# Performance work log

Hardware: AMD Instinct MI355X
Metric: run time of the kernel (lower is better)

Reference implementation:

```python
import jax, jax.numpy as jnp
import numpy as np

B, L, D, H = 4, 2048, 1024, 16
HD = D // H

def setup_inputs() -> dict:
    key = jax.random.key(0)
    k1, k2, k3, k4 = jax.random.split(key, 4)
    return {
        "Q": jax.random.normal(k1, (B, L, D), dtype=jnp.float32),
        "K": jax.random.normal(k2, (B, L, D), dtype=jnp.float32),
        "V": jax.random.normal(k3, (B, L, D), dtype=jnp.float32),
        "W_out": jax.random.normal(k4, (D, D), dtype=jnp.float32) * (1.0 / np.sqrt(D)),
        "b_out": jnp.zeros((D,), dtype=jnp.float32),
    }

def reference(Q, K, V, W_out, b_out):
    b, l, d = Q.shape
    h, hd = H, d // H
    q = Q.reshape(b, l, h, hd)
    k = K.reshape(b, l, h, hd)
    v = V.reshape(b, l, h, hd)
    # energy: [b, h, q, k]
    energy = jnp.einsum('nqhd,nkhd->nhqk', q, k)
    # NOTE: original scales by sqrt(embed_dim), not sqrt(head_dim)
    attn = jax.nn.softmax(energy / jnp.sqrt(jnp.float32(d)), axis=-1)
    out = jnp.einsum('nhql,nlhd->nqhd', attn, v).reshape(b, l, d)
    # torch nn.Linear: x @ W.T + b
    return out @ W_out.T + b_out
```

## Files before the change

kernel.cpp:

```cpp
#include <hip/hip_runtime.h>
#include <hip/hip_bf16.h>


#define B_  4
#define L_  2048
#define D_  1024
#define H_  16

typedef float  f32x4  __attribute__((ext_vector_type(4)));
typedef short  bf16x8 __attribute__((ext_vector_type(8)));
typedef short  bf16x4 __attribute__((ext_vector_type(4)));

__device__ inline unsigned short f2bf(float x) {
    union { float f; unsigned u; } v; v.f = x;
    unsigned r = v.u + 0x7FFFu + ((v.u >> 16) & 1u);
    return (unsigned short)(r >> 16);
}
__device__ inline unsigned pack_rne2(float lo, float hi) {
    return (unsigned)f2bf(lo) | ((unsigned)f2bf(hi) << 16);
}
__device__ inline unsigned pack_trunc2(float lo, float hi) {
    union { float f; unsigned u; } a, b; a.f = lo; b.f = hi;
    return (a.u >> 16) | (b.u & 0xFFFF0000u);
}
__device__ inline float fast_exp2(float x) {
#if __has_builtin(__builtin_amdgcn_exp2f)
    return __builtin_amdgcn_exp2f(x);
#else
    return exp2f(x);
#endif
}
__device__ inline bf16x8 pack8s(float4 a, float4 b, float s) {
    bf16x8 r;
    r[0] = (short)f2bf(a.x * s); r[1] = (short)f2bf(a.y * s);
    r[2] = (short)f2bf(a.z * s); r[3] = (short)f2bf(a.w * s);
    r[4] = (short)f2bf(b.x * s); r[5] = (short)f2bf(b.y * s);
    r[6] = (short)f2bf(b.z * s); r[7] = (short)f2bf(b.w * s);
    return r;
}
__device__ inline void gld16(const void* g, void* l) {
    __builtin_amdgcn_global_load_lds(
        (const __attribute__((address_space(1))) void*)g,
        (__attribute__((address_space(3))) void*)l, 16, 0, 0);
}

__global__ __launch_bounds__(256) void convw_kernel(const float* __restrict__ W,
                                                    unsigned short* __restrict__ Wb) {
    int i = (blockIdx.x * 256 + threadIdx.x) * 4;
    float4 v = *(const float4*)&W[i];
    bf16x4 o;
    o[0] = (short)f2bf(v.x); o[1] = (short)f2bf(v.y);
    o[2] = (short)f2bf(v.z); o[3] = (short)f2bf(v.w);
    *(bf16x4*)&Wb[i] = o;
}

__global__ __launch_bounds__(256) void convk_kernel(const float* __restrict__ K,
                                                    unsigned short* __restrict__ Kb) {
    int o = blockIdx.x * 256 + threadIdx.x;
    int d8 = o & 7; int h = (o >> 3) & 15; int key = (o >> 7) & 2047; int b = o >> 18;
    size_t base = ((size_t)(b * L_ + key) * H_ + h) * 64;
    const float* p = K + base + d8 * 8;
    float4 a = *(const float4*)p, c = *(const float4*)(p + 4);
    bf16x8 r;
    r[0] = (short)f2bf(a.x); r[1] = (short)f2bf(a.y); r[2] = (short)f2bf(a.z); r[3] = (short)f2bf(a.w);
    r[4] = (short)f2bf(c.x); r[5] = (short)f2bf(c.y); r[6] = (short)f2bf(c.z); r[7] = (short)f2bf(c.w);
    *(bf16x8*)&Kb[base + ((d8 * 8) ^ ((key & 7) * 8))] = r;
}

__global__ __launch_bounds__(256) void convv_kernel(const float* __restrict__ V,
                                                    unsigned short* __restrict__ Vb) {
    __shared__ unsigned short T[64 * 80];
    int tid = threadIdx.x;
    int kb_ = blockIdx.x & 31, bh = blockIdx.x >> 5;
    int b = bh >> 4, h = bh & 15, k0 = kb_ * 64;
    int key2 = tid & 31, dg = tid >> 5;
    const float* pa = V + ((size_t)(b * L_ + k0 + 2 * key2) * H_ + h) * 64 + dg * 8;
    const float* pb = pa + H_ * 64;
    float4 a0 = *(const float4*)pa, a1 = *(const float4*)(pa + 4);
    float4 b0 = *(const float4*)pb, b1 = *(const float4*)(pb + 4);
    #pragma unroll
    for (int j = 0; j < 4; ++j)
        *(unsigned*)&T[(dg * 8 + j) * 80 + 2 * key2] =
            pack_rne2(((const float*)&a0)[j], ((const float*)&b0)[j]);
    #pragma unroll
    for (int j = 0; j < 4; ++j)
        *(unsigned*)&T[(dg * 8 + 4 + j) * 80 + 2 * key2] =
            pack_rne2(((const float*)&a1)[j], ((const float*)&b1)[j]);
    __syncthreads();
    #pragma unroll
    for (int i = 0; i < 2; ++i) {
        int c = i * 256 + tid; int d = c >> 3, ch = c & 7;
        bf16x8 v = *(const bf16x8*)&T[d * 80 + ch * 8];
        *(bf16x8*)&Vb[((size_t)(b * H_ + h) * 64 + d) * L_ + k0 + ((ch ^ (d & 7)) * 8)] = v;
    }
}

__global__ __launch_bounds__(256, 3) void attn_kernel(const float* __restrict__ Qg,
                                                      const unsigned short* __restrict__ Kb,
                                                      const unsigned short* __restrict__ Vb,
                                                      unsigned short* __restrict__ Og) {
    __shared__ unsigned short Ks[2][64 * 64];
    __shared__ unsigned short Vt[2][64 * 64];
    __shared__ unsigned short Pw[4][32 * 64];

    const int tid  = threadIdx.x;
    const int w    = tid >> 6;
    const int lane = tid & 63;
    const int l16  = lane & 15;
    const int quad = lane >> 4;

    const int x   = blockIdx.x;
    const int idx = x >> 3;
    const int bh  = (x & 7) * 8 + (idx & 7);
    const int qb  = idx >> 3;
    const int bz  = bh >> 4;
    const int h   = bh & 15;
    const int q0  = qb * 128;

    const float qscale = 0.04508422f;
    bf16x8 aq[2][2];
    #pragma unroll
    for (int qt = 0; qt < 2; ++qt) {
        const int qrow = q0 + w * 32 + qt * 16 + l16;
        const float* qp = Qg + ((size_t)(bz * L_ + qrow)) * D_ + h * 64 + quad * 8;
        aq[qt][0] = pack8s(*(const float4*)qp,        *(const float4*)(qp + 4),  qscale);
        aq[qt][1] = pack8s(*(const float4*)(qp + 32), *(const float4*)(qp + 36), qscale);
    }

    f32x4 o[2][4];
    float lsum[2] = {0.f, 0.f};
    #pragma unroll
    for (int qt = 0; qt < 2; ++qt)
        #pragma unroll
        for (int i = 0; i < 4; ++i) o[qt][i] = (f32x4){0.f, 0.f, 0.f, 0.f};

    const unsigned short* Kbh = Kb + ((size_t)bz * L_ * H_ + h) * 64;
    const unsigned short* Vbh = Vb + (size_t)(bz * H_ + h) * 64 * L_;
    unsigned short* PwF = &Pw[0][0];
    const int sw = (l16 & 7) * 8;

    #define ISSUE(T, BUF)                                                           \
        {                                                                           \
            int k0_ = (T) * 64;                                                     \
            _Pragma("unroll")                                                       \
            for (int i = 0; i < 2; ++i) {                                           \
                int c = i * 256 + tid; int rr = c >> 3, jj = c & 7;                 \
                gld16(Kbh + (size_t)(k0_ + rr) * (H_ * 64) + jj * 8,                \
                      (char*)Ks[BUF] + (i * 256 + w * 64) * 16);                    \
                gld16(Vbh + (size_t)rr * L_ + k0_ + jj * 8,                         \
                      (char*)Vt[BUF] + (i * 256 + w * 64) * 16);                    \
            }                                                                       \
        }

    ISSUE(0, 0)

    for (int t = 0; t < 32; ++t) {
        __syncthreads();
        if (t < 31) ISSUE(t + 1, (t + 1) & 1)
        const unsigned short* ks = Ks[t & 1];
        const unsigned short* vt = Vt[t & 1];

        f32x4 s[2][4];
        #pragma unroll
        for (int nt = 0; nt < 4; ++nt) {
            bf16x8 k0f = *(const bf16x8*)&ks[(nt * 16 + l16) * 64 + ((quad * 8) ^ sw)];
            bf16x8 k1f = *(const bf16x8*)&ks[(nt * 16 + l16) * 64 + ((32 + quad * 8) ^ sw)];
            #pragma unroll
            for (int qt = 0; qt < 2; ++qt) {
                f32x4 z = (f32x4){0.f, 0.f, 0.f, 0.f};
                z = __builtin_amdgcn_mfma_f32_16x16x32_bf16(k0f, aq[qt][0], z, 0, 0, 0);
                s[qt][nt] = __builtin_amdgcn_mfma_f32_16x16x32_bf16(k1f, aq[qt][1], z, 0, 0, 0);
            }
        }

        #pragma unroll
        for (int qt = 0; qt < 2; ++qt) {
            int prow = (w * 32 + qt * 16 + l16) * 64;
            #pragma unroll
            for (int nt = 0; nt < 4; ++nt) {
                float p0 = fast_exp2(s[qt][nt][0]), p1 = fast_exp2(s[qt][nt][1]);
                float p2 = fast_exp2(s[qt][nt][2]), p3 = fast_exp2(s[qt][nt][3]);
                lsum[qt] += (p0 + p1) + (p2 + p3);
                int cb = nt * 16 + quad * 4;
                *(unsigned*)&PwF[prow + ((cb)     ^ sw)] = pack_trunc2(p0, p1);
                *(unsigned*)&PwF[prow + ((cb + 2) ^ sw)] = pack_trunc2(p2, p3);
            }
        }

        bf16x8 pav[2][2];
        #pragma unroll
        for (int qt = 0; qt < 2; ++qt) {
            int prow = (w * 32 + qt * 16 + l16) * 64;
            pav[qt][0] = *(const bf16x8*)&PwF[prow + ((quad * 8)      ^ sw)];
            pav[qt][1] = *(const bf16x8*)&PwF[prow + ((32 + quad * 8) ^ sw)];
        }
        #pragma unroll
        for (int dt = 0; dt < 4; ++dt) {
            bf16x8 v0 = *(const bf16x8*)&vt[(dt * 16 + l16) * 64 + ((quad * 8)      ^ sw)];
            bf16x8 v1 = *(const bf16x8*)&vt[(dt * 16 + l16) * 64 + ((32 + quad * 8) ^ sw)];
            #pragma unroll
            for (int qt = 0; qt < 2; ++qt) {
                o[qt][dt] = __builtin_amdgcn_mfma_f32_16x16x32_bf16(pav[qt][0], v0, o[qt][dt], 0, 0, 0);
                o[qt][dt] = __builtin_amdgcn_mfma_f32_16x16x32_bf16(pav[qt][1], v1, o[qt][dt], 0, 0, 0);
            }
        }
    }

    float tot[2];
    #pragma unroll
    for (int qt = 0; qt < 2; ++qt) {
        float v = lsum[qt];
        v += __shfl_xor(v, 16); v += __shfl_xor(v, 32);
        tot[qt] = v;
    }
    #pragma unroll
    for (int qt = 0; qt < 2; ++qt)
        #pragma unroll
        for (int r = 0; r < 4; ++r) {
            float tv  = __shfl(tot[qt], quad * 4 + r);
            float inv = 1.0f / tv;
            int q = q0 + w * 32 + qt * 16 + quad * 4 + r;
            size_t rowb = ((size_t)(bz * L_ + q)) * D_ + h * 64;
            #pragma unroll
            for (int dt = 0; dt < 4; ++dt)
                Og[rowb + dt * 16 + l16] = f2bf(o[qt][dt][r] * inv);
        }
}

__global__ __launch_bounds__(256, 2) void proj_kernel(const unsigned short* __restrict__ Og,
                                                      const unsigned short* __restrict__ Wb,
                                                      const float* __restrict__ bias,
                                                      float* __restrict__ Yg) {
    __shared__ unsigned short As[2][128 * 32];
    __shared__ unsigned short Bs[2][128 * 32];

    const int tid  = threadIdx.x;
    const int w    = tid >> 6;
    const int lane = tid & 63;
    const int l16  = lane & 15;
    const int quad = lane >> 4;
    const int wm   = w & 1, wn = w >> 1;

    const int m0 = blockIdx.x * 128;
    const int n0 = blockIdx.y * 128;

    f32x4 acc[4][4];
    #pragma unroll
    for (int i = 0; i < 4; ++i)
        #pragma unroll
        for (int j = 0; j < 4; ++j) acc[i][j] = (f32x4){0.f, 0.f, 0.f, 0.f};

    #define PISSUE(T, BUF)                                                          \
        {                                                                           \
            int kt_ = (T) * 32;                                                     \
            _Pragma("unroll")                                                       \
            for (int i = 0; i < 2; ++i) {                                           \
                int c = i * 256 + tid; int row = c >> 2, q4 = c & 3;                \
                gld16(&Og[(size_t)(m0 + row) * 1024 + kt_ + q4 * 8],                \
                      (char*)As[BUF] + (i * 256 + w * 64) * 16);                    \
                gld16(&Wb[(size_t)(n0 + row) * 1024 + kt_ + q4 * 8],                \
                      (char*)Bs[BUF] + (i * 256 + w * 64) * 16);                    \
            }                                                                       \
        }

    PISSUE(0, 0)

    for (int t = 0; t < 32; ++t) {
        __syncthreads();
        if (t < 31) PISSUE(t + 1, (t + 1) & 1)
        const unsigned short* as = As[t & 1];
        const unsigned short* bs = Bs[t & 1];

        bf16x8 a[4], b[4];
        #pragma unroll
        for (int mt = 0; mt < 4; ++mt)
            a[mt] = *(const bf16x8*)&as[(wm * 64 + mt * 16 + l16) * 32 + quad * 8];
        #pragma unroll
        for (int nt = 0; nt < 4; ++nt)
            b[nt] = *(const bf16x8*)&bs[(wn * 64 + nt * 16 + l16) * 32 + quad * 8];
        #pragma unroll
        for (int mt = 0; mt < 4; ++mt)
            #pragma unroll
            for (int nt = 0; nt < 4; ++nt)
                acc[mt][nt] = __builtin_amdgcn_mfma_f32_16x16x32_bf16(a[mt], b[nt], acc[mt][nt], 0, 0, 0);
    }

    #pragma unroll
    for (int mt = 0; mt < 4; ++mt)
        #pragma unroll
        for (int nt = 0; nt < 4; ++nt) {
            int e = n0 + wn * 64 + nt * 16 + l16;
            float bv = bias[e];
            #pragma unroll
            for (int r = 0; r < 4; ++r) {
                int m = m0 + wm * 64 + mt * 16 + quad * 4 + r;
                Yg[(size_t)m * 1024 + e] = acc[mt][nt][r] + bv;
            }
        }
}

extern "C" void kernel_launch(void* const* d_in, const int* in_sizes, int n_in,
                              void* d_out, int out_size, void* d_ws, size_t ws_size,
                              hipStream_t stream) {
    const float* Q    = (const float*)d_in[0];
    const float* K    = (const float*)d_in[1];
    const float* V    = (const float*)d_in[2];
    const float* W    = (const float*)d_in[3];
    const float* bias = (const float*)d_in[4];
    float* Y = (float*)d_out;

    unsigned short* Og = (unsigned short*)d_ws;
    unsigned short* Wb = (unsigned short*)((char*)d_ws + (size_t)16 * 1024 * 1024);
    unsigned short* Kb = (unsigned short*)d_out;
    unsigned short* Vb = Kb + (size_t)B_ * H_ * L_ * 64;

    convw_kernel<<<D_ * D_ / (256 * 4), 256, 0, stream>>>(W, Wb);
    convk_kernel<<<B_ * L_ * H_ * 8 / 256, 256, 0, stream>>>(K, Kb);
    convv_kernel<<<B_ * H_ * (L_ / 64), 256, 0, stream>>>(V, Vb);
    attn_kernel<<<B_ * H_ * (L_ / 128), 256, 0, stream>>>(Q, Kb, Vb, Og);
    dim3 pg(B_ * L_ / 128, D_ / 128);
    proj_kernel<<<pg, 256, 0, stream>>>(Og, Wb, bias, Y);
}
```

Baseline: 265.9 us.

## Shuffle P in registers, raise attn occupancy, widen proj K-tile, rework V transpose

The attention kernel drops its shared-memory P staging buffer and rebuilds the bf16 P fragments for the PV MFMA with cross-lane shuffles, which frees LDS and lets the occupancy hint rise from 3 to 4 blocks. The projection GEMM doubles its K tile to 64 with an XOR-swizzled LDS layout, halving the number of barriers and loop iterations. The V conversion kernel now reads one float4 per key row and writes scalar bf16 values into a narrower padded LDS tile. The trade-off is more shuffle instructions in the attention kernel, register pressure under the tighter occupancy bound, and twice the LDS per proj block.

```diff
diff --git a/kernel.cpp b/kernel.cpp
--- a/kernel.cpp
+++ b/kernel.cpp
@@ -15,9 +15,6 @@
     union { float f; unsigned u; } v; v.f = x;
     unsigned r = v.u + 0x7FFFu + ((v.u >> 16) & 1u);
     return (unsigned short)(r >> 16);
-}
-__device__ inline unsigned pack_rne2(float lo, float hi) {
-    return (unsigned)f2bf(lo) | ((unsigned)f2bf(hi) << 16);
 }
 __device__ inline unsigned pack_trunc2(float lo, float hi) {
     union { float f; unsigned u; } a, b; a.f = lo; b.f = hi;
@@ -69,39 +66,37 @@
 
 __global__ __launch_bounds__(256) void convv_kernel(const float* __restrict__ V,
                                                     unsigned short* __restrict__ Vb) {
-    __shared__ unsigned short T[64 * 80];
+    __shared__ __align__(16) unsigned short T[64 * 72];
     int tid = threadIdx.x;
     int kb_ = blockIdx.x & 31, bh = blockIdx.x >> 5;
     int b = bh >> 4, h = bh & 15, k0 = kb_ * 64;
-    int key2 = tid & 31, dg = tid >> 5;
-    const float* pa = V + ((size_t)(b * L_ + k0 + 2 * key2) * H_ + h) * 64 + dg * 8;
-    const float* pb = pa + H_ * 64;
-    float4 a0 = *(const float4*)pa, a1 = *(const float4*)(pa + 4);
-    float4 b0 = *(const float4*)pb, b1 = *(const float4*)(pb + 4);
-    #pragma unroll
-    for (int j = 0; j < 4; ++j)
-        *(unsigned*)&T[(dg * 8 + j) * 80 + 2 * key2] =
-            pack_rne2(((const float*)&a0)[j], ((const float*)&b0)[j]);
-    #pragma unroll
-    for (int j = 0; j < 4; ++j)
-        *(unsigned*)&T[(dg * 8 + 4 + j) * 80 + 2 * key2] =
-            pack_rne2(((const float*)&a1)[j], ((const float*)&b1)[j]);
+    int kl = tid >> 4;
+    int d4 = (tid & 15) * 4;
+    #pragma unroll
+    for (int pp = 0; pp < 4; ++pp) {
+        int key = pp * 16 + kl;
+        const float* p = V + ((size_t)(b * L_ + k0 + key)) * D_ + h * 64 + d4;
+        float4 v = *(const float4*)p;
+        T[(d4 + 0) * 72 + key] = f2bf(v.x);
+        T[(d4 + 1) * 72 + key] = f2bf(v.y);
+        T[(d4 + 2) * 72 + key] = f2bf(v.z);
+        T[(d4 + 3) * 72 + key] = f2bf(v.w);
+    }
     __syncthreads();
     #pragma unroll
     for (int i = 0; i < 2; ++i) {
         int c = i * 256 + tid; int d = c >> 3, ch = c & 7;
-        bf16x8 v = *(const bf16x8*)&T[d * 80 + ch * 8];
+        bf16x8 v = *(const bf16x8*)&T[d * 72 + ch * 8];
         *(bf16x8*)&Vb[((size_t)(b * H_ + h) * 64 + d) * L_ + k0 + ((ch ^ (d & 7)) * 8)] = v;
     }
 }
 
-__global__ __launch_bounds__(256, 3) void attn_kernel(const float* __restrict__ Qg,
+__global__ __launch_bounds__(256, 4) void attn_kernel(const float* __restrict__ Qg,
                                                       const unsigned short* __restrict__ Kb,
                                                       const unsigned short* __restrict__ Vb,
                                                       unsigned short* __restrict__ Og) {
     __shared__ unsigned short Ks[2][64 * 64];
     __shared__ unsigned short Vt[2][64 * 64];
-    __shared__ unsigned short Pw[4][32 * 64];
 
     const int tid  = threadIdx.x;
     const int w    = tid >> 6;
@@ -136,8 +131,10 @@
 
     const unsigned short* Kbh = Kb + ((size_t)bz * L_ * H_ + h) * 64;
     const unsigned short* Vbh = Vb + (size_t)(bz * H_ + h) * 64 * L_;
-    unsigned short* PwF = &Pw[0][0];
     const int sw = (l16 & 7) * 8;
+    const int hi = quad >> 1;
+    const int i0 = (quad & 1) * 32 + l16;
+    const int i1 = i0 + 16;
 
     #define ISSUE(T, BUF)                                                           \
         {                                                                           \
@@ -173,27 +170,36 @@
             }
         }
 
-        #pragma unroll
-        for (int qt = 0; qt < 2; ++qt) {
-            int prow = (w * 32 + qt * 16 + l16) * 64;
+        unsigned packed[2][4][2];
+        #pragma unroll
+        for (int qt = 0; qt < 2; ++qt)
             #pragma unroll
             for (int nt = 0; nt < 4; ++nt) {
                 float p0 = fast_exp2(s[qt][nt][0]), p1 = fast_exp2(s[qt][nt][1]);
                 float p2 = fast_exp2(s[qt][nt][2]), p3 = fast_exp2(s[qt][nt][3]);
                 lsum[qt] += (p0 + p1) + (p2 + p3);
-                int cb = nt * 16 + quad * 4;
-                *(unsigned*)&PwF[prow + ((cb)     ^ sw)] = pack_trunc2(p0, p1);
-                *(unsigned*)&PwF[prow + ((cb + 2) ^ sw)] = pack_trunc2(p2, p3);
-            }
-        }
+                packed[qt][nt][0] = pack_trunc2(p0, p1);
+                packed[qt][nt][1] = pack_trunc2(p2, p3);
+            }
 
         bf16x8 pav[2][2];
         #pragma unroll
         for (int qt = 0; qt < 2; ++qt) {
-            int prow = (w * 32 + qt * 16 + l16) * 64;
-            pav[qt][0] = *(const bf16x8*)&PwF[prow + ((quad * 8)      ^ sw)];
-            pav[qt][1] = *(const bf16x8*)&PwF[prow + ((32 + quad * 8) ^ sw)];
-        }
+            union { int i[4]; bf16x8 v; } u0, u1;
+            #pragma unroll
+            for (int fp = 0; fp < 4; ++fp) {
+                int src = (fp & 2) ? i1 : i0;
+                int f   = fp & 1;
+                int lo0 = __shfl((int)packed[qt][0][f], src);
+                int hi0 = __shfl((int)packed[qt][1][f], src);
+                u0.i[fp] = hi ? hi0 : lo0;
+                int lo1 = __shfl((int)packed[qt][2][f], src);
+                int hi1 = __shfl((int)packed[qt][3][f], src);
+                u1.i[fp] = hi ? hi1 : lo1;
+            }
+            pav[qt][0] = u0.v; pav[qt][1] = u1.v;
+        }
+
         #pragma unroll
         for (int dt = 0; dt < 4; ++dt) {
             bf16x8 v0 = *(const bf16x8*)&vt[(dt * 16 + l16) * 64 + ((quad * 8)      ^ sw)];
@@ -231,8 +237,8 @@
                                                       const unsigned short* __restrict__ Wb,
                                                       const float* __restrict__ bias,
                                                       float* __restrict__ Yg) {
-    __shared__ unsigned short As[2][128 * 32];
-    __shared__ unsigned short Bs[2][128 * 32];
+    __shared__ unsigned short As[2][128 * 64];
+    __shared__ unsigned short Bs[2][128 * 64];
 
     const int tid  = threadIdx.x;
     const int w    = tid >> 6;
@@ -252,37 +258,45 @@
 
     #define PISSUE(T, BUF)                                                          \
         {                                                                           \
-            int kt_ = (T) * 32;                                                     \
+            int kt_ = (T) * 64;                                                     \
             _Pragma("unroll")                                                       \
-            for (int i = 0; i < 2; ++i) {                                           \
-                int c = i * 256 + tid; int row = c >> 2, q4 = c & 3;                \
-                gld16(&Og[(size_t)(m0 + row) * 1024 + kt_ + q4 * 8],                \
+            for (int i = 0; i < 4; ++i) {                                           \
+                int c = i * 256 + tid; int row = c >> 3, p = c & 7;                 \
+                int j = p ^ (row & 7);                                              \
+                gld16(&Og[(size_t)(m0 + row) * 1024 + kt_ + j * 8],                 \
                       (char*)As[BUF] + (i * 256 + w * 64) * 16);                    \
-                gld16(&Wb[(size_t)(n0 + row) * 1024 + kt_ + q4 * 8],                \
+                gld16(&Wb[(size_t)(n0 + row) * 1024 + kt_ + j * 8],                 \
                       (char*)Bs[BUF] + (i * 256 + w * 64) * 16);                    \
             }                                                                       \
         }
 
     PISSUE(0, 0)
 
-    for (int t = 0; t < 32; ++t) {
+    for (int t = 0; t < 16; ++t) {
         __syncthreads();
-        if (t < 31) PISSUE(t + 1, (t + 1) & 1)
+        if (t < 15) PISSUE(t + 1, (t + 1) & 1)
         const unsigned short* as = As[t & 1];
         const unsigned short* bs = Bs[t & 1];
 
-        bf16x8 a[4], b[4];
-        #pragma unroll
-        for (int mt = 0; mt < 4; ++mt)
-            a[mt] = *(const bf16x8*)&as[(wm * 64 + mt * 16 + l16) * 32 + quad * 8];
-        #pragma unroll
-        for (int nt = 0; nt < 4; ++nt)
-            b[nt] = *(const bf16x8*)&bs[(wn * 64 + nt * 16 + l16) * 32 + quad * 8];
-        #pragma unroll
-        for (int mt = 0; mt < 4; ++mt)
-            #pragma unroll
-            for (int nt = 0; nt < 4; ++nt)
-                acc[mt][nt] = __builtin_amdgcn_mfma_f32_16x16x32_bf16(a[mt], b[nt], acc[mt][nt], 0, 0, 0);
+        #pragma unroll
+        for (int ksq = 0; ksq < 2; ++ksq) {
+            bf16x8 a[4], b[4];
+            #pragma unroll
+            for (int mt = 0; mt < 4; ++mt) {
+                int row = wm * 64 + mt * 16 + l16;
+                a[mt] = *(const bf16x8*)&as[row * 64 + (((ksq * 4 + quad) ^ (l16 & 7)) * 8)];
+            }
+            #pragma unroll
+            for (int nt = 0; nt < 4; ++nt) {
+                int row = wn * 64 + nt * 16 + l16;
+                b[nt] = *(const bf16x8*)&bs[row * 64 + (((ksq * 4 + quad) ^ (l16 & 7)) * 8)];
+            }
+            #pragma unroll
+            for (int mt = 0; mt < 4; ++mt)
+                #pragma unroll
+                for (int nt = 0; nt < 4; ++nt)
+                    acc[mt][nt] = __builtin_amdgcn_mfma_f32_16x16x32_bf16(a[mt], b[nt], acc[mt][nt], 0, 0, 0);
+        }
     }
 
     #pragma unroll
```

After: 260.5 us. -2.1%, faster.
